# Kernel optimization log

Measured on AMD Instinct MI355X. Metric: run time of the kernel, lower is better.

Reference implementation:

```python
import jax, jax.numpy as jnp
import numpy as np

B, L, C, H, W = 1, 16, 16, 128, 256  # L = T_chunk = K_chunk (single chunk, causal)
DECAY = 0.1  # decay_val


def setup_inputs() -> dict:
    key = jax.random.key(0)
    k1, k2 = jax.random.split(key)
    img = jax.random.normal(k1, (B, L, C, H, W), jnp.float32)
    # flows in normalized [-1,1] grid units; keep displacements modest
    cum_flow = jax.random.normal(k2, (B, L, 2, H, W), jnp.float32) * 0.1
    t = jnp.arange(L)
    mask = (t[:, None] >= t[None, :]).astype(jnp.float32)          # causal [T,K]
    decay_dist = jnp.abs(t[:, None] - t[None, :]).astype(jnp.float32)  # [T,K]
    return {"img": img, "cum_flow": cum_flow, "mask": mask, "decay_dist": decay_dist}


def _bilinear_sample(img, gx, gy):
    # img: [B,K,C,H,W]; gx, gy: [B,K,H,W] in normalized [-1,1] coords.
    # x wraps around (periodic), y clamps -- matching the kernel's index handling.
    ix = (gx + 1.0) * (W * 0.5) - 0.5
    iy = (gy + 1.0) * (H * 0.5) - 0.5
    x0 = jnp.floor(ix)
    y0 = jnp.floor(iy)
    wx = ix - x0  # fractional weights
    wy = iy - y0
    x0i = x0.astype(jnp.int32)
    y0i = y0.astype(jnp.int32)
    x0r = jnp.mod(x0i, W)
    x1r = jnpp = jnp.mod(x0i + 1, W)
    y0c = jnp.clip(y0i, 0, H - 1)
    y1c = jnp.clip(y0i + 1, 0, H - 1)

    K = img.shape[1]
    imgf = img.reshape(B, K, C, H * W)

    def gather(yy, xx):
        idx = (yy * W + xx).reshape(B, K, 1, H * W)  # broadcast over C
        return jnp.take_along_axis(imgf, idx, axis=-1).reshape(B, K, C, H, W)

    va = gather(y0c, x0r)  # (y0, x0)
    vb = gather(y1c, x0r)  # (y1, x0)
    vc = gather(y0c, x1r)  # (y0, x1)
    vd = gather(y1c, x1r)  # (y1, x1)
    wx_ = wx[:, :, None]   # [B,K,1,H,W]
    wy_ = wy[:, :, None]
    return (va * (1.0 - wx_) * (1.0 - wy_) + vb * (1.0 - wx_) * wy_
            + vc * wx_ * (1.0 - wy_) + vd * wx_ * wy_)


def reference(img, cum_flow, mask, decay_dist):
    # base grid (align_corners=False style pixel centers)
    base_x = (jnp.arange(W, dtype=jnp.float32) * (2.0 / W) - 1.0 + 1.0 / W)[None, None, :]  # [1,1,W]
    base_y = (jnp.arange(H, dtype=jnp.float32) * (2.0 / H) - 1.0 + 1.0 / H)[None, :, None]  # [1,H,1]

    weights = mask * jnp.exp(-DECAY * decay_dist)  # [T,K] decay-weighted causal mask
    fx = cum_flow[:, :, 0]  # [B,L,H,W]
    fy = cum_flow[:, :, 1]

    def step(carry, inp):
        ft_x, ft_y, w_row = inp  # ft_*: [B,H,W]; w_row: [K]
        gx = base_x[None] + (ft_x[:, None] - fx)  # [B,K,H,W]
        gy = base_y[None] + (ft_y[:, None] - fy)
        gx = jnp.mod(gx + 1.0, 2.0) - 1.0          # wrap x into [-1,1)
        sampled = _bilinear_sample(img, gx, gy)    # [B,K,C,H,W]
        out_t = jnp.einsum('k,bkchw->bchw', w_row, sampled)
        return carry, out_t

    xs = (jnp.moveaxis(fx, 1, 0), jnp.moveaxis(fy, 1, 0), weights)  # over t
    _, outs = jax.lax.scan(step, 0.0, xs)          # [T,B,C,H,W]
    return jnp.moveaxis(outs, 0, 1)                # [B,T,C,H,W]
```

## Files before the change

kernel.cpp:

```cpp
#include <hip/hip_runtime.h>

constexpr int Lc = 16;
constexpr int Cc = 16;
constexpr int Hc = 128;
constexpr int Wc = 256;
constexpr float DECAYc = 0.1f;
constexpr int HWc = Hc * Wc;

__global__ __launch_bounds__(256) void transpose_chlast(
    const float* __restrict__ img, float* __restrict__ imgT)
{
    const int tid = threadIdx.x;
    const int wq = tid >> 2;
    const int q  = tid & 3;
    const int pix = blockIdx.x * 64 + wq;
    const int k = blockIdx.y;

    const float* __restrict__ src = img + (size_t)k * Cc * HWc + pix;
    float4 v;
    v.x = src[(4 * q + 0) * HWc];
    v.y = src[(4 * q + 1) * HWc];
    v.z = src[(4 * q + 2) * HWc];
    v.w = src[(4 * q + 3) * HWc];
    float4* __restrict__ dst = (float4*)(imgT + ((size_t)k * HWc + pix) * Cc);
    dst[q] = v;
}

__global__ __launch_bounds__(256) void gridsample_chlast_q(
    const float* __restrict__ imgT,
    const float* __restrict__ cum_flow,
    const float* __restrict__ mask,
    const float* __restrict__ decay,
    float* __restrict__ out)
{
    const int tid = threadIdx.x;
    const int wq = tid >> 2;
    const int q  = tid & 3;
    const int bx = blockIdx.x;
    const int h  = bx >> 2;
    const int w  = (bx & 3) * 64 + wq;
    const int t  = blockIdx.y;

    const int pix = h * Wc + w;

    const float base_x = w * (2.0f / Wc) - 1.0f + 1.0f / Wc;
    const float base_y = h * (2.0f / Hc) - 1.0f + 1.0f / Hc;

    const float fxt = cum_flow[(t * 2 + 0) * HWc + pix];
    const float fyt = cum_flow[(t * 2 + 1) * HWc + pix];

    float4 acc = {0.0f, 0.0f, 0.0f, 0.0f};

    for (int k = 0; k < t; ++k) {
        const float wkt = mask[t * Lc + k] * __expf(-DECAYc * decay[t * Lc + k]);

        const float fxk = cum_flow[(k * 2 + 0) * HWc + pix];
        const float fyk = cum_flow[(k * 2 + 1) * HWc + pix];

        float gx = base_x + (fxt - fxk);
        const float gy = base_y + (fyt - fyk);

        {
            float m = gx + 1.0f;
            m -= 2.0f * floorf(m * 0.5f);
            gx = m - 1.0f;
        }

        const float ix = (gx + 1.0f) * (Wc * 0.5f) - 0.5f;
        const float iy = (gy + 1.0f) * (Hc * 0.5f) - 0.5f;

        const float x0f = floorf(ix);
        const float y0f = floorf(iy);
        const float wx = ix - x0f;
        const float wy = iy - y0f;

        const int x0 = (int)x0f;
        const int y0 = (int)y0f;
        const int x0r = x0 & (Wc - 1);
        const int x1r = (x0 + 1) & (Wc - 1);
        const int y0c = min(max(y0, 0), Hc - 1);
        const int y1c = min(max(y0 + 1, 0), Hc - 1);

        const float a00 = wkt * (1.0f - wx) * (1.0f - wy);
        const float a01 = wkt * (1.0f - wx) * wy;
        const float a10 = wkt * wx * (1.0f - wy);
        const float a11 = wkt * wx * wy;

        const float* __restrict__ bk = imgT + (size_t)k * HWc * Cc;
        const float4 v00 = ((const float4*)(bk + (y0c * Wc + x0r) * Cc))[q];
        const float4 v10 = ((const float4*)(bk + (y0c * Wc + x1r) * Cc))[q];
        const float4 v01 = ((const float4*)(bk + (y1c * Wc + x0r) * Cc))[q];
        const float4 v11 = ((const float4*)(bk + (y1c * Wc + x1r) * Cc))[q];

        acc.x += a00 * v00.x + a10 * v10.x + a01 * v01.x + a11 * v11.x;
        acc.y += a00 * v00.y + a10 * v10.y + a01 * v01.y + a11 * v11.y;
        acc.z += a00 * v00.z + a10 * v10.z + a01 * v01.z + a11 * v11.z;
        acc.w += a00 * v00.w + a10 * v10.w + a01 * v01.w + a11 * v11.w;
    }

    {
        const float4 idv = ((const float4*)(imgT + ((size_t)t * HWc + pix) * Cc))[q];
        acc.x += idv.x;
        acc.y += idv.y;
        acc.z += idv.z;
        acc.w += idv.w;
    }

    float* __restrict__ op = out + (size_t)t * Cc * HWc + (size_t)(4 * q) * HWc + pix;
    op[0 * HWc] = acc.x;
    op[1 * HWc] = acc.y;
    op[2 * HWc] = acc.z;
    op[3 * HWc] = acc.w;
}

__global__ __launch_bounds__(256) void gridsample_warp_acc(
    const float* __restrict__ img, const float* __restrict__ cum_flow,
    const float* __restrict__ mask, const float* __restrict__ decay,
    float* __restrict__ out)
{
    const int w = threadIdx.x, h = blockIdx.x, t = blockIdx.y;
    const int pix = h * Wc + w;
    const float base_x = w * (2.0f / Wc) - 1.0f + 1.0f / Wc;
    const float base_y = h * (2.0f / Hc) - 1.0f + 1.0f / Hc;
    const float fxt = cum_flow[(t * 2 + 0) * HWc + pix];
    const float fyt = cum_flow[(t * 2 + 1) * HWc + pix];
    float acc[Cc];
#pragma unroll
    for (int c = 0; c < Cc; ++c) acc[c] = 0.0f;
    for (int k = 0; k <= t; ++k) {
        const float wkt = mask[t * Lc + k] * __expf(-DECAYc * decay[t * Lc + k]);
        const float fxk = cum_flow[(k * 2 + 0) * HWc + pix];
        const float fyk = cum_flow[(k * 2 + 1) * HWc + pix];
        float gx = base_x + (fxt - fxk);
        const float gy = base_y + (fyt - fyk);
        float m = gx + 1.0f;
        m -= 2.0f * floorf(m * 0.5f);
        gx = m - 1.0f;
        const float ix = (gx + 1.0f) * (Wc * 0.5f) - 0.5f;
        const float iy = (gy + 1.0f) * (Hc * 0.5f) - 0.5f;
        const float x0f = floorf(ix), y0f = floorf(iy);
        const float wx = ix - x0f, wy = iy - y0f;
        const int x0 = (int)x0f, y0 = (int)y0f;
        const int x0r = x0 & (Wc - 1), x1r = (x0 + 1) & (Wc - 1);
        const int y0c = min(max(y0, 0), Hc - 1), y1c = min(max(y0 + 1, 0), Hc - 1);
        const float a00 = wkt * (1.0f - wx) * (1.0f - wy);
        const float a01 = wkt * (1.0f - wx) * wy;
        const float a10 = wkt * wx * (1.0f - wy);
        const float a11 = wkt * wx * wy;
        const int o00 = y0c * Wc + x0r, o01 = y1c * Wc + x0r;
        const int o10 = y0c * Wc + x1r, o11 = y1c * Wc + x1r;
        const float* __restrict__ ik = img + (size_t)k * Cc * HWc;
#pragma unroll
        for (int c = 0; c < Cc; ++c) {
            const float* __restrict__ p = ik + c * HWc;
            acc[c] += p[o00] * a00 + p[o01] * a01 + p[o10] * a10 + p[o11] * a11;
        }
    }
    float* __restrict__ op = out + (size_t)t * Cc * HWc + pix;
#pragma unroll
    for (int c = 0; c < Cc; ++c) op[c * HWc] = acc[c];
}

extern "C" void kernel_launch(void* const* d_in, const int* in_sizes, int n_in,
                              void* d_out, int out_size, void* d_ws, size_t ws_size,
                              hipStream_t stream) {
    const float* img      = (const float*)d_in[0];
    const float* cum_flow = (const float*)d_in[1];
    const float* mask     = (const float*)d_in[2];
    const float* decay    = (const float*)d_in[3];
    float* out = (float*)d_out;

    const size_t needed = (size_t)Lc * HWc * Cc * sizeof(float);
    if (ws_size >= needed) {
        float* imgT = (float*)d_ws;
        dim3 tgrid(HWc / 64, Lc, 1);
        transpose_chlast<<<tgrid, 256, 0, stream>>>(img, imgT);
        dim3 grid(Hc * (Wc / 64), Lc, 1);
        gridsample_chlast_q<<<grid, 256, 0, stream>>>(imgT, cum_flow, mask, decay, out);
    } else {
        dim3 grid(Hc, Lc, 1);
        gridsample_warp_acc<<<grid, Wc, 0, stream>>>(img, cum_flow, mask, decay, out);
    }
}
```

Measured before the change: 185.2 us.

## Merge all output timesteps per thread and stage transpose through LDS

```diff
diff --git a/kernel.cpp b/kernel.cpp
--- a/kernel.cpp
+++ b/kernel.cpp
@@ -7,26 +7,46 @@
 constexpr float DECAYc = 0.1f;
 constexpr int HWc = Hc * Wc;
 
-__global__ __launch_bounds__(256) void transpose_chlast(
+__global__ __launch_bounds__(256) void transpose_chlast_lds(
     const float* __restrict__ img, float* __restrict__ imgT)
 {
+    __shared__ float tile[256 * 17];
     const int tid = threadIdx.x;
-    const int wq = tid >> 2;
-    const int q  = tid & 3;
-    const int pix = blockIdx.x * 64 + wq;
     const int k = blockIdx.y;
-
-    const float* __restrict__ src = img + (size_t)k * Cc * HWc + pix;
-    float4 v;
-    v.x = src[(4 * q + 0) * HWc];
-    v.y = src[(4 * q + 1) * HWc];
-    v.z = src[(4 * q + 2) * HWc];
-    v.w = src[(4 * q + 3) * HWc];
-    float4* __restrict__ dst = (float4*)(imgT + ((size_t)k * HWc + pix) * Cc);
-    dst[q] = v;
-}
-
-__global__ __launch_bounds__(256) void gridsample_chlast_q(
+    const int px0 = blockIdx.x * 256;
+
+    {
+        const int c = tid >> 4;
+        const int g = tid & 15;
+        const float* __restrict__ src = img + (size_t)k * Cc * HWc + (size_t)c * HWc + px0;
+#pragma unroll
+        for (int r = 0; r < 4; ++r) {
+            const int p4 = 4 * (g + 16 * r);
+            const float4 v = *(const float4*)(src + p4);
+            tile[(p4 + 0) * 17 + c] = v.x;
+            tile[(p4 + 1) * 17 + c] = v.y;
+            tile[(p4 + 2) * 17 + c] = v.z;
+            tile[(p4 + 3) * 17 + c] = v.w;
+        }
+    }
+    __syncthreads();
+    {
+        const int q = tid & 3;
+        const int pb = tid >> 2;
+#pragma unroll
+        for (int r = 0; r < 4; ++r) {
+            const int px = pb + 64 * r;
+            float4 o;
+            o.x = tile[px * 17 + 4 * q + 0];
+            o.y = tile[px * 17 + 4 * q + 1];
+            o.z = tile[px * 17 + 4 * q + 2];
+            o.w = tile[px * 17 + 4 * q + 3];
+            ((float4*)(imgT + ((size_t)k * HWc + px0 + px) * Cc))[q] = o;
+        }
+    }
+}
+
+__global__ __launch_bounds__(256) void gridsample_tmerge(
     const float* __restrict__ imgT,
     const float* __restrict__ cum_flow,
     const float* __restrict__ mask,
@@ -37,80 +57,90 @@
     const int wq = tid >> 2;
     const int q  = tid & 3;
     const int bx = blockIdx.x;
-    const int h  = bx >> 2;
-    const int w  = (bx & 3) * 64 + wq;
-    const int t  = blockIdx.y;
+    const int band = bx & 7;
+    const int sub  = bx >> 3;
+    const int h = band * 16 + (sub >> 2);
+    const int w = (sub & 3) * 64 + wq;
 
     const int pix = h * Wc + w;
 
     const float base_x = w * (2.0f / Wc) - 1.0f + 1.0f / Wc;
     const float base_y = h * (2.0f / Hc) - 1.0f + 1.0f / Hc;
 
-    const float fxt = cum_flow[(t * 2 + 0) * HWc + pix];
-    const float fyt = cum_flow[(t * 2 + 1) * HWc + pix];
-
-    float4 acc = {0.0f, 0.0f, 0.0f, 0.0f};
-
-    for (int k = 0; k < t; ++k) {
-        const float wkt = mask[t * Lc + k] * __expf(-DECAYc * decay[t * Lc + k]);
-
+    float fxs[Lc], fys[Lc];
+#pragma unroll
+    for (int t = 0; t < Lc; ++t) {
+        fxs[t] = cum_flow[(t * 2 + 0) * HWc + pix];
+        fys[t] = cum_flow[(t * 2 + 1) * HWc + pix];
+    }
+
+    float4 acc[Lc];
+#pragma unroll
+    for (int t = 0; t < Lc; ++t) acc[t] = make_float4(0.f, 0.f, 0.f, 0.f);
+
+    for (int k = 0; k < Lc; ++k) {
         const float fxk = cum_flow[(k * 2 + 0) * HWc + pix];
         const float fyk = cum_flow[(k * 2 + 1) * HWc + pix];
-
-        float gx = base_x + (fxt - fxk);
-        const float gy = base_y + (fyt - fyk);
-
-        {
-            float m = gx + 1.0f;
-            m -= 2.0f * floorf(m * 0.5f);
-            gx = m - 1.0f;
-        }
-
-        const float ix = (gx + 1.0f) * (Wc * 0.5f) - 0.5f;
-        const float iy = (gy + 1.0f) * (Hc * 0.5f) - 0.5f;
-
-        const float x0f = floorf(ix);
-        const float y0f = floorf(iy);
-        const float wx = ix - x0f;
-        const float wy = iy - y0f;
-
-        const int x0 = (int)x0f;
-        const int y0 = (int)y0f;
-        const int x0r = x0 & (Wc - 1);
-        const int x1r = (x0 + 1) & (Wc - 1);
-        const int y0c = min(max(y0, 0), Hc - 1);
-        const int y1c = min(max(y0 + 1, 0), Hc - 1);
-
-        const float a00 = wkt * (1.0f - wx) * (1.0f - wy);
-        const float a01 = wkt * (1.0f - wx) * wy;
-        const float a10 = wkt * wx * (1.0f - wy);
-        const float a11 = wkt * wx * wy;
-
+        const float4 idv = ((const float4*)(imgT + ((size_t)k * HWc + pix) * Cc))[q];
         const float* __restrict__ bk = imgT + (size_t)k * HWc * Cc;
-        const float4 v00 = ((const float4*)(bk + (y0c * Wc + x0r) * Cc))[q];
-        const float4 v10 = ((const float4*)(bk + (y0c * Wc + x1r) * Cc))[q];
-        const float4 v01 = ((const float4*)(bk + (y1c * Wc + x0r) * Cc))[q];
-        const float4 v11 = ((const float4*)(bk + (y1c * Wc + x1r) * Cc))[q];
-
-        acc.x += a00 * v00.x + a10 * v10.x + a01 * v01.x + a11 * v11.x;
-        acc.y += a00 * v00.y + a10 * v10.y + a01 * v01.y + a11 * v11.y;
-        acc.z += a00 * v00.z + a10 * v10.z + a01 * v01.z + a11 * v11.z;
-        acc.w += a00 * v00.w + a10 * v10.w + a01 * v01.w + a11 * v11.w;
-    }
-
-    {
-        const float4 idv = ((const float4*)(imgT + ((size_t)t * HWc + pix) * Cc))[q];
-        acc.x += idv.x;
-        acc.y += idv.y;
-        acc.z += idv.z;
-        acc.w += idv.w;
-    }
-
-    float* __restrict__ op = out + (size_t)t * Cc * HWc + (size_t)(4 * q) * HWc + pix;
-    op[0 * HWc] = acc.x;
-    op[1 * HWc] = acc.y;
-    op[2 * HWc] = acc.z;
-    op[3 * HWc] = acc.w;
+
+#pragma unroll
+        for (int t = 0; t < Lc; ++t) {
+            if (t == k) {
+                acc[t].x += idv.x; acc[t].y += idv.y;
+                acc[t].z += idv.z; acc[t].w += idv.w;
+            } else if (t > k) {
+                const float wkt = mask[t * Lc + k] *
+                                  __expf(-DECAYc * decay[t * Lc + k]);
+
+                float gx = base_x + (fxs[t] - fxk);
+                const float gy = base_y + (fys[t] - fyk);
+
+                float m = gx + 1.0f;
+                m -= 2.0f * floorf(m * 0.5f);
+                gx = m - 1.0f;
+
+                const float ix = (gx + 1.0f) * (Wc * 0.5f) - 0.5f;
+                const float iy = (gy + 1.0f) * (Hc * 0.5f) - 0.5f;
+
+                const float x0f = floorf(ix);
+                const float y0f = floorf(iy);
+                const float wx = ix - x0f;
+                const float wy = iy - y0f;
+
+                const int x0 = (int)x0f;
+                const int y0 = (int)y0f;
+                const int x0r = x0 & (Wc - 1);
+                const int x1r = (x0 + 1) & (Wc - 1);
+                const int y0c = min(max(y0, 0), Hc - 1);
+                const int y1c = min(max(y0 + 1, 0), Hc - 1);
+
+                const float a00 = wkt * (1.0f - wx) * (1.0f - wy);
+                const float a01 = wkt * (1.0f - wx) * wy;
+                const float a10 = wkt * wx * (1.0f - wy);
+                const float a11 = wkt * wx * wy;
+
+                const float4 v00 = ((const float4*)(bk + (y0c * Wc + x0r) * Cc))[q];
+                const float4 v10 = ((const float4*)(bk + (y0c * Wc + x1r) * Cc))[q];
+                const float4 v01 = ((const float4*)(bk + (y1c * Wc + x0r) * Cc))[q];
+                const float4 v11 = ((const float4*)(bk + (y1c * Wc + x1r) * Cc))[q];
+
+                acc[t].x += a00 * v00.x + a10 * v10.x + a01 * v01.x + a11 * v11.x;
+                acc[t].y += a00 * v00.y + a10 * v10.y + a01 * v01.y + a11 * v11.y;
+                acc[t].z += a00 * v00.z + a10 * v10.z + a01 * v01.z + a11 * v11.z;
+                acc[t].w += a00 * v00.w + a10 * v10.w + a01 * v01.w + a11 * v11.w;
+            }
+        }
+    }
+
+#pragma unroll
+    for (int t = 0; t < Lc; ++t) {
+        float* __restrict__ op = out + ((size_t)t * Cc + 4 * q) * HWc + pix;
+        op[0 * HWc] = acc[t].x;
+        op[1 * HWc] = acc[t].y;
+        op[2 * HWc] = acc[t].z;
+        op[3 * HWc] = acc[t].w;
+    }
 }
 
 __global__ __launch_bounds__(256) void gridsample_warp_acc(
@@ -173,10 +203,9 @@
     const size_t needed = (size_t)Lc * HWc * Cc * sizeof(float);
     if (ws_size >= needed) {
         float* imgT = (float*)d_ws;
-        dim3 tgrid(HWc / 64, Lc, 1);
-        transpose_chlast<<<tgrid, 256, 0, stream>>>(img, imgT);
-        dim3 grid(Hc * (Wc / 64), Lc, 1);
-        gridsample_chlast_q<<<grid, 256, 0, stream>>>(imgT, cum_flow, mask, decay, out);
+        dim3 tgrid(HWc / 256, Lc, 1);
+        transpose_chlast_lds<<<tgrid, 256, 0, stream>>>(img, imgT);
+        gridsample_tmerge<<<512, 256, 0, stream>>>(imgT, cum_flow, mask, decay, out);
     } else {
         dim3 grid(Hc, Lc, 1);
         gridsample_warp_acc<<<grid, Wc, 0, stream>>>(img, cum_flow, mask, decay, out);
```

After: 158.2 us. 14.6% less time.

## Give each thread four interleaved timesteps to balance the causal load and reuse flow loads

Applied to the files above, without the earlier changes.

```diff
diff --git a/kernel.cpp b/kernel.cpp
--- a/kernel.cpp
+++ b/kernel.cpp
@@ -11,106 +11,126 @@
     const float* __restrict__ img, float* __restrict__ imgT)
 {
     const int tid = threadIdx.x;
+    const int q  = tid & 3;
     const int wq = tid >> 2;
-    const int q  = tid & 3;
-    const int pix = blockIdx.x * 64 + wq;
-    const int k = blockIdx.y;
-
-    const float* __restrict__ src = img + (size_t)k * Cc * HWc + pix;
-    float4 v;
-    v.x = src[(4 * q + 0) * HWc];
-    v.y = src[(4 * q + 1) * HWc];
-    v.z = src[(4 * q + 2) * HWc];
-    v.w = src[(4 * q + 3) * HWc];
-    float4* __restrict__ dst = (float4*)(imgT + ((size_t)k * HWc + pix) * Cc);
-    dst[q] = v;
-}
-
-__global__ __launch_bounds__(256) void gridsample_chlast_q(
+    const int kf  = blockIdx.x >> 6;
+    const int seg = blockIdx.x & 63;
+    const int px0 = seg * 512;
+    const float* __restrict__ srcb = img + (size_t)kf * Cc * HWc;
+#pragma unroll
+    for (int r = 0; r < 8; ++r) {
+        const int px = px0 + r * 64 + wq;
+        float4 v;
+        v.x = srcb[(4 * q + 0) * HWc + px];
+        v.y = srcb[(4 * q + 1) * HWc + px];
+        v.z = srcb[(4 * q + 2) * HWc + px];
+        v.w = srcb[(4 * q + 3) * HWc + px];
+        ((float4*)(imgT + ((size_t)kf * HWc + px) * Cc))[q] = v;
+    }
+}
+
+__global__ __launch_bounds__(256, 6) void gridsample_tquarter(
     const float* __restrict__ imgT,
     const float* __restrict__ cum_flow,
     const float* __restrict__ mask,
     const float* __restrict__ decay,
     float* __restrict__ out)
 {
+    __shared__ float wtab[Lc * Lc];
     const int tid = threadIdx.x;
+    if (tid < Lc * Lc)
+        wtab[tid] = mask[tid] * __expf(-DECAYc * decay[tid]);
+    __syncthreads();
+
+    const int q  = tid & 3;
     const int wq = tid >> 2;
-    const int q  = tid & 3;
-    const int bx = blockIdx.x;
-    const int h  = bx >> 2;
-    const int w  = (bx & 3) * 64 + wq;
-    const int t  = blockIdx.y;
-
+    const int b = blockIdx.x;
+    const int band = b & 7;
+    const int r    = (b >> 3) & 3;
+    const int sub  = b >> 5;
+    const int h = band * 16 + (sub >> 2);
+    const int w = (sub & 3) * 64 + wq;
     const int pix = h * Wc + w;
 
     const float base_x = w * (2.0f / Wc) - 1.0f + 1.0f / Wc;
     const float base_y = h * (2.0f / Hc) - 1.0f + 1.0f / Hc;
 
-    const float fxt = cum_flow[(t * 2 + 0) * HWc + pix];
-    const float fyt = cum_flow[(t * 2 + 1) * HWc + pix];
-
-    float4 acc = {0.0f, 0.0f, 0.0f, 0.0f};
-
-    for (int k = 0; k < t; ++k) {
-        const float wkt = mask[t * Lc + k] * __expf(-DECAYc * decay[t * Lc + k]);
-
+    float sx1[4], sy1[4];
+#pragma unroll
+    for (int i = 0; i < 4; ++i) {
+        const int t = 4 * i + r;
+        sx1[i] = base_x + cum_flow[(t * 2 + 0) * HWc + pix] + 1.0f;
+        sy1[i] = base_y + cum_flow[(t * 2 + 1) * HWc + pix] + 1.0f;
+    }
+
+    float4 acc[4];
+#pragma unroll
+    for (int i = 0; i < 4; ++i) acc[i] = make_float4(0.f, 0.f, 0.f, 0.f);
+
+    const int kmax = 12 + r;
+    for (int k = 0; k <= kmax; ++k) {
         const float fxk = cum_flow[(k * 2 + 0) * HWc + pix];
         const float fyk = cum_flow[(k * 2 + 1) * HWc + pix];
-
-        float gx = base_x + (fxt - fxk);
-        const float gy = base_y + (fyt - fyk);
-
-        {
-            float m = gx + 1.0f;
+        const float* __restrict__ bk = imgT + (size_t)k * HWc * Cc;
+
+#pragma unroll
+        for (int i = 0; i < 4; ++i) {
+            const int t = 4 * i + r;
+            if (t < k) continue;
+            if (t == k) {
+                const float4 idv = ((const float4*)(bk + pix * Cc))[q];
+                acc[i].x += idv.x; acc[i].y += idv.y;
+                acc[i].z += idv.z; acc[i].w += idv.w;
+                continue;
+            }
+            const float wkt = wtab[t * Lc + k];
+
+            float m = sx1[i] - fxk;
             m -= 2.0f * floorf(m * 0.5f);
-            gx = m - 1.0f;
+            const float ix = m * (Wc * 0.5f) - 0.5f;
+            const float iy = (sy1[i] - fyk) * (Hc * 0.5f) - 0.5f;
+
+            const float x0f = floorf(ix);
+            const float y0f = floorf(iy);
+            const float wx = ix - x0f;
+            const float wy = iy - y0f;
+
+            const int x0 = (int)x0f;
+            const int y0 = (int)y0f;
+            const int x0r = x0 & (Wc - 1);
+            const int x1r = (x0 + 1) & (Wc - 1);
+            const int y0c = min(max(y0, 0), Hc - 1);
+            const int y1c = min(max(y0 + 1, 0), Hc - 1);
+
+            const float wb = wkt * wy;
+            const float wa = wkt - wb;
+            const float omx = 1.0f - wx;
+            const float a00 = wa * omx;
+            const float a10 = wa * wx;
+            const float a01 = wb * omx;
+            const float a11 = wb * wx;
+
+            const float4 v00 = ((const float4*)(bk + (y0c * Wc + x0r) * Cc))[q];
+            const float4 v10 = ((const float4*)(bk + (y0c * Wc + x1r) * Cc))[q];
+            const float4 v01 = ((const float4*)(bk + (y1c * Wc + x0r) * Cc))[q];
+            const float4 v11 = ((const float4*)(bk + (y1c * Wc + x1r) * Cc))[q];
+
+            acc[i].x += a00 * v00.x + a10 * v10.x + a01 * v01.x + a11 * v11.x;
+            acc[i].y += a00 * v00.y + a10 * v10.y + a01 * v01.y + a11 * v11.y;
+            acc[i].z += a00 * v00.z + a10 * v10.z + a01 * v01.z + a11 * v11.z;
+            acc[i].w += a00 * v00.w + a10 * v10.w + a01 * v01.w + a11 * v11.w;
         }
-
-        const float ix = (gx + 1.0f) * (Wc * 0.5f) - 0.5f;
-        const float iy = (gy + 1.0f) * (Hc * 0.5f) - 0.5f;
-
-        const float x0f = floorf(ix);
-        const float y0f = floorf(iy);
-        const float wx = ix - x0f;
-        const float wy = iy - y0f;
-
-        const int x0 = (int)x0f;
-        const int y0 = (int)y0f;
-        const int x0r = x0 & (Wc - 1);
-        const int x1r = (x0 + 1) & (Wc - 1);
-        const int y0c = min(max(y0, 0), Hc - 1);
-        const int y1c = min(max(y0 + 1, 0), Hc - 1);
-
-        const float a00 = wkt * (1.0f - wx) * (1.0f - wy);
-        const float a01 = wkt * (1.0f - wx) * wy;
-        const float a10 = wkt * wx * (1.0f - wy);
-        const float a11 = wkt * wx * wy;
-
-        const float* __restrict__ bk = imgT + (size_t)k * HWc * Cc;
-        const float4 v00 = ((const float4*)(bk + (y0c * Wc + x0r) * Cc))[q];
-        const float4 v10 = ((const float4*)(bk + (y0c * Wc + x1r) * Cc))[q];
-        const float4 v01 = ((const float4*)(bk + (y1c * Wc + x0r) * Cc))[q];
-        const float4 v11 = ((const float4*)(bk + (y1c * Wc + x1r) * Cc))[q];
-
-        acc.x += a00 * v00.x + a10 * v10.x + a01 * v01.x + a11 * v11.x;
-        acc.y += a00 * v00.y + a10 * v10.y + a01 * v01.y + a11 * v11.y;
-        acc.z += a00 * v00.z + a10 * v10.z + a01 * v01.z + a11 * v11.z;
-        acc.w += a00 * v00.w + a10 * v10.w + a01 * v01.w + a11 * v11.w;
-    }
-
-    {
-        const float4 idv = ((const float4*)(imgT + ((size_t)t * HWc + pix) * Cc))[q];
-        acc.x += idv.x;
-        acc.y += idv.y;
-        acc.z += idv.z;
-        acc.w += idv.w;
-    }
-
-    float* __restrict__ op = out + (size_t)t * Cc * HWc + (size_t)(4 * q) * HWc + pix;
-    op[0 * HWc] = acc.x;
-    op[1 * HWc] = acc.y;
-    op[2 * HWc] = acc.z;
-    op[3 * HWc] = acc.w;
+    }
+
+#pragma unroll
+    for (int i = 0; i < 4; ++i) {
+        const int t = 4 * i + r;
+        float* __restrict__ op = out + ((size_t)t * Cc + 4 * q) * HWc + pix;
+        op[0 * HWc] = acc[i].x;
+        op[1 * HWc] = acc[i].y;
+        op[2 * HWc] = acc[i].z;
+        op[3 * HWc] = acc[i].w;
+    }
 }
 
 __global__ __launch_bounds__(256) void gridsample_warp_acc(
@@ -173,10 +193,8 @@
     const size_t needed = (size_t)Lc * HWc * Cc * sizeof(float);
     if (ws_size >= needed) {
         float* imgT = (float*)d_ws;
-        dim3 tgrid(HWc / 64, Lc, 1);
-        transpose_chlast<<<tgrid, 256, 0, stream>>>(img, imgT);
-        dim3 grid(Hc * (Wc / 64), Lc, 1);
-        gridsample_chlast_q<<<grid, 256, 0, stream>>>(imgT, cum_flow, mask, decay, out);
+        transpose_chlast<<<dim3(64 * Lc), 256, 0, stream>>>(img, imgT);
+        gridsample_tquarter<<<dim3(2048), 256, 0, stream>>>(imgT, cum_flow, mask, decay, out);
     } else {
         dim3 grid(Hc, Lc, 1);
         gridsample_warp_acc<<<grid, Wc, 0, stream>>>(img, cum_flow, mask, decay, out);
```

Measured after the change: 188.4 us. About the same (+1.7%).
